# Kernel optimization log

Hardware: AMD Instinct MI355X
Metric: run time of the kernel (lower is better)

The kernel has to match this reference:

```python
import jax, jax.numpy as jnp
import numpy as np

B, S, D_IN = 4, 2048, 1024
D_OUT, H = 1024, 16
HD = D_OUT // H  # head_dim = 64

def setup_inputs() -> dict:
    key = jax.random.key(0)
    ks = jax.random.split(key, 6)
    scale_in = 1.0 / np.sqrt(D_IN)
    scale_out = 1.0 / np.sqrt(D_OUT)
    return {
        "x": jax.random.normal(ks[0], (B, S, D_IN), dtype=jnp.float32),
        "Wq": jax.random.uniform(ks[1], (D_OUT, D_IN), jnp.float32, -scale_in, scale_in),
        "Wk": jax.random.uniform(ks[2], (D_OUT, D_IN), jnp.float32, -scale_in, scale_in),
        "Wv": jax.random.uniform(ks[3], (D_OUT, D_IN), jnp.float32, -scale_in, scale_in),
        "Wo": jax.random.uniform(ks[4], (D_OUT, D_OUT), jnp.float32, -scale_out, scale_out),
        "bo": jax.random.uniform(ks[5], (D_OUT,), jnp.float32, -scale_out, scale_out),
    }

def reference(x, Wq, Wk, Wv, Wo, bo):
    b, s, _ = x.shape
    # projections (nn.Linear: x @ W.T), split into heads -> [b, h, s, hd]
    def proj(W):
        return jnp.einsum('bsd,ed->bse', x, W).reshape(b, s, H, HD).transpose(0, 2, 1, 3)
    q, k, v = proj(Wq), proj(Wk), proj(Wv)
    # full score matrix [b, h, s, s] with causal mask, scaled softmax
    scores = jnp.einsum('bhqd,bhkd->bhqk', q, k)
    causal = jnp.tril(jnp.ones((s, s), dtype=bool))
    scores = jnp.where(causal, scores, -jnp.inf)
    attn = jax.nn.softmax(scores / np.sqrt(HD), axis=-1)
    # dropout p=0.0 -> identity
    ctx = jnp.einsum('bhqk,bhkd->bqhd', attn, v).reshape(b, s, D_OUT)
    return jnp.einsum('bsd,ed->bse', ctx, Wo) + bo
```

## Files before the change

kernel.cpp:

```cpp
#include <hip/hip_runtime.h>
#include <cstdint>
#include <cstddef>

#define S_LEN   2048
#define D_MODEL 1024
#define N_HEADS 16
#define HEAD_DIM 64
#define BATCH   4
#define M_ROWS  (BATCH * S_LEN)

typedef _Float16 half8  __attribute__((ext_vector_type(8)));
typedef _Float16 half4v __attribute__((ext_vector_type(4)));
typedef float    float4v __attribute__((ext_vector_type(4)));

#define AS1 __attribute__((address_space(1)))
#define AS3 __attribute__((address_space(3)))

#define QSCL 0.1803368801111832f

__device__ __forceinline__ int swz(int row, int byteInRow) {
    return row * 128 + ((((byteInRow >> 4) ^ (row & 7)) << 4)) + (byteInRow & 15);
}

__device__ __forceinline__ int vperm(int a) {
    return (a & 0x20) | ((a & 0x0C) << 1) | ((a & 0x10) >> 2) | (a & 3);
}

__global__ __launch_bounds__(256) void cvt_all(const float* __restrict__ x,
                                               const float* __restrict__ wq,
                                               const float* __restrict__ wk,
                                               const float* __restrict__ wv,
                                               const float* __restrict__ wo,
                                               _Float16* __restrict__ dst) {
    const int NX = M_ROWS * D_MODEL / 4;
    const int NW = D_MODEL * D_MODEL / 4;
    int i = blockIdx.x * 256 + threadIdx.x;
    int j = i;
    const float4v* src;
    if (j < NX) src = (const float4v*)x;
    else {
        j -= NX;
        if (j < NW) src = (const float4v*)wq;
        else { j -= NW;
            if (j < NW) src = (const float4v*)wk;
            else { j -= NW;
                if (j < NW) src = (const float4v*)wv;
                else { j -= NW; src = (const float4v*)wo; }
            }
        }
    }
    float4v v = src[j];
    half4v h;
    h[0] = (_Float16)v[0]; h[1] = (_Float16)v[1];
    h[2] = (_Float16)v[2]; h[3] = (_Float16)v[3];
    ((half4v*)dst)[i] = h;
}

#define GK   1024
#define GNT  16
#define BUFB 49152
#define GEMM_LDS (3 * BUFB)

template <int MODE>
__global__ __launch_bounds__(512, 2) void gemm8p(const _Float16* __restrict__ A,
                                                 const _Float16* __restrict__ Bw,
                                                 _Float16* __restrict__ O1,
                                                 _Float16* __restrict__ O2,
                                                 _Float16* __restrict__ O3,
                                                 float* __restrict__ Of,
                                                 const float* __restrict__ bias,
                                                 int N) {
    extern __shared__ char smem[];

    const int tid  = threadIdx.x;
    const int wave = tid >> 6;
    const int lane = tid & 63;
    const int quad = lane >> 4;
    const int l16  = lane & 15;
    const int wm   = wave >> 1;
    const int wn   = wave & 1;

    const int rowBase = blockIdx.x * 256;
    const int colBase = blockIdx.y * 128;

    const int srow = tid >> 3;
    const int csw  = ((tid & 7) ^ (srow & 7)) * 8;
    const _Float16* aS[4];
    const _Float16* bS[2];
#pragma unroll
    for (int i = 0; i < 4; ++i)
        aS[i] = A + (size_t)(rowBase + i * 64 + srow) * GK + csw;
#pragma unroll
    for (int j = 0; j < 2; ++j)
        bS[j] = Bw + (size_t)(colBase + j * 64 + srow) * GK + csw;
    const int dstOff = tid * 16;

    auto stage = [&](int kt, int part) {
        char* base = smem + (kt % 3) * BUFB;
        const size_t ko = (size_t)kt * 64;
        if (part == 0) {
            __builtin_amdgcn_global_load_lds((const AS1 void*)(aS[0] + ko),
                (AS3 void*)(base + 0 * 8192 + dstOff), 16, 0, 0);
            __builtin_amdgcn_global_load_lds((const AS1 void*)(aS[1] + ko),
                (AS3 void*)(base + 1 * 8192 + dstOff), 16, 0, 0);
            __builtin_amdgcn_global_load_lds((const AS1 void*)(bS[0] + ko),
                (AS3 void*)(base + 32768 + dstOff), 16, 0, 0);
        } else {
            __builtin_amdgcn_global_load_lds((const AS1 void*)(aS[2] + ko),
                (AS3 void*)(base + 2 * 8192 + dstOff), 16, 0, 0);
            __builtin_amdgcn_global_load_lds((const AS1 void*)(aS[3] + ko),
                (AS3 void*)(base + 3 * 8192 + dstOff), 16, 0, 0);
            __builtin_amdgcn_global_load_lds((const AS1 void*)(bS[1] + ko),
                (AS3 void*)(base + 32768 + 8192 + dstOff), 16, 0, 0);
        }
    };

    const int aRow = (wm * 64 + l16) * 128;
    const int bRow = (wn * 64 + l16) * 128;
    int swzk[2];
    swzk[0] = ((quad)     ^ (l16 & 7)) << 4;
    swzk[1] = ((quad + 4) ^ (l16 & 7)) << 4;

    float4v acc[4][4] = {};

    stage(0, 0); stage(0, 1); stage(1, 0); stage(1, 1);
    asm volatile("s_waitcnt vmcnt(6)" ::: "memory");
    __builtin_amdgcn_s_barrier();

#pragma unroll
    for (int kt = 0; kt < GNT; ++kt) {
        const char* Ab = smem + (kt % 3) * BUFB;
        const char* Bb = Ab + 32768;
#pragma unroll
        for (int ks = 0; ks < 2; ++ks) {
            half8 af[4], bf[4];
#pragma unroll
            for (int mi = 0; mi < 4; ++mi)
                af[mi] = *(const half8*)(Ab + aRow + mi * 2048 + swzk[ks]);
#pragma unroll
            for (int ni = 0; ni < 4; ++ni)
                bf[ni] = *(const half8*)(Bb + bRow + ni * 2048 + swzk[ks]);
            if (kt + 2 < GNT) stage(kt + 2, ks);
            __builtin_amdgcn_s_barrier();
            asm volatile("s_waitcnt lgkmcnt(0)" ::: "memory");
            __builtin_amdgcn_sched_barrier(0);
            __builtin_amdgcn_s_setprio(1);
#pragma unroll
            for (int mi = 0; mi < 4; ++mi)
#pragma unroll
                for (int ni = 0; ni < 4; ++ni)
                    acc[mi][ni] = __builtin_amdgcn_mfma_f32_16x16x32_f16(
                        af[mi], bf[ni], acc[mi][ni], 0, 0, 0);
            __builtin_amdgcn_s_setprio(0);
            if (ks == 1) {
                if (kt + 2 < GNT) {
                    asm volatile("s_waitcnt vmcnt(6)" ::: "memory");
                } else if (kt + 1 < GNT) {
                    asm volatile("s_waitcnt vmcnt(0)" ::: "memory");
                }
            }
            __builtin_amdgcn_s_barrier();
        }
    }

    const int rowOff = wm * 64;
    const int colOff = wn * 64;
#pragma unroll
    for (int mi = 0; mi < 4; ++mi)
#pragma unroll
        for (int ni = 0; ni < 4; ++ni) {
            const int col = colBase + colOff + ni * 16 + l16;
#pragma unroll
            for (int i = 0; i < 4; ++i) {
                const int row = rowBase + rowOff + mi * 16 + quad * 4 + i;
                float v = acc[mi][ni][i];
                if (MODE == 0) {
                    int b_ = row >> 11, s_ = row & 2047;
                    int proj = col >> 10, d = col & 1023;
                    int h_ = d >> 6, hd = d & 63;
                    if (proj == 2) {
                        int sp = (s_ & ~63) | vperm(s_ & 63);
                        O3[(((size_t)(b_ * 16 + h_) * 64 + hd) << 11) + sp] = (_Float16)v;
                    } else {
                        _Float16* dst = proj ? O2 : O1;
                        if (proj == 0) v *= QSCL;
                        dst[(((size_t)(b_ * 16 + h_) * 2048 + s_) << 6) + hd] = (_Float16)v;
                    }
                } else {
                    Of[(size_t)row * N + col] = v + bias[col];
                }
            }
        }
}

template <bool MASKED>
__device__ __forceinline__ void qk_sm(const half8 qf[2],
                                      const _Float16* __restrict__ Ks,
                                      int krow0, int qt, int quad, int c,
                                      half8 (&pf)[2], float4v& ol, half8 ones) {
    float4v sT[4] = {};
    __builtin_amdgcn_s_setprio(1);
#pragma unroll
    for (int nt = 0; nt < 4; ++nt)
#pragma unroll
        for (int ks = 0; ks < 2; ++ks) {
            half8 kf = *(const half8*)((const char*)Ks + swz(nt * 16 + c, ks * 64 + quad * 16));
            sT[nt] = __builtin_amdgcn_mfma_f32_16x16x32_f16(kf, qf[ks], sT[nt], 0, 0, 0);
        }
    __builtin_amdgcn_s_setprio(0);

    const int qrow = qt + c;
#pragma unroll
    for (int kk = 0; kk < 2; ++kk) {
        float e[2][4];
#pragma unroll
        for (int jh = 0; jh < 2; ++jh) {
            const int nt = 2 * kk + jh;
#pragma unroll
            for (int i = 0; i < 4; ++i) {
                float ev = __builtin_amdgcn_exp2f(sT[nt][i]);
                if (MASKED)
                    ev = (krow0 + nt * 16 + quad * 4 + i <= qrow) ? ev : 0.0f;
                e[jh][i] = ev;
            }
        }
        auto p0 = __builtin_amdgcn_cvt_pkrtz(e[0][0], e[0][1]);
        auto p1 = __builtin_amdgcn_cvt_pkrtz(e[0][2], e[0][3]);
        auto p2 = __builtin_amdgcn_cvt_pkrtz(e[1][0], e[1][1]);
        auto p3 = __builtin_amdgcn_cvt_pkrtz(e[1][2], e[1][3]);
        half8 pfv;
        pfv[0] = p0[0]; pfv[1] = p0[1]; pfv[2] = p1[0]; pfv[3] = p1[1];
        pfv[4] = p2[0]; pfv[5] = p2[1]; pfv[6] = p3[0]; pfv[7] = p3[1];
        pf[kk] = pfv;
        ol = __builtin_amdgcn_mfma_f32_16x16x32_f16(pfv, ones, ol, 0, 0, 0);
    }
}

__global__ __launch_bounds__(256, 4) void attn_flash10(const _Float16* __restrict__ Q,
                                                       const _Float16* __restrict__ Kg,
                                                       const _Float16* __restrict__ Vt,
                                                       _Float16* __restrict__ Ctx) {
    __shared__ __align__(16) _Float16 Ks[2 * 64 * 64];
    __shared__ __align__(16) _Float16 Vs[2 * 64 * 64];

    const int tid  = threadIdx.x;
    const int wave = tid >> 6;
    const int lane = tid & 63;
    const int quad = lane >> 4;
    const int c    = lane & 15;

    const int h    = blockIdx.x;
    const int y    = blockIdx.y;
    const int bb   = blockIdx.z;
    const int hp   = (y < 8) ? y : 23 - y;
    const int pair = hp >> 1;
    const int hf   = hp & 1;

    const int qA   = pair * 128 + hf * 64 + wave * 16;
    const int qB   = (15 - pair) * 128 + hf * 64 + wave * 16;
    const int nkbB = (15 - pair) * 2 + hf + 1;

    const _Float16* Qb  = Q  + ((size_t)(bb * 16 + h) << 17);
    const _Float16* Kb  = Kg + ((size_t)(bb * 16 + h) << 17);
    const _Float16* Vtb = Vt + ((size_t)(bb * 16 + h) << 17);

    half8 qfA[2], qfB[2];
    {
        const _Float16* qa = Qb + (size_t)(qA + c) * 64;
        qfA[0] = *(const half8*)(qa + quad * 8);
        qfA[1] = *(const half8*)(qa + 32 + quad * 8);
        const _Float16* qb = Qb + (size_t)(qB + c) * 64;
        qfB[0] = *(const half8*)(qb + quad * 8);
        qfB[1] = *(const half8*)(qb + 32 + quad * 8);
    }

    size_t koff[2], voff[2];
#pragma unroll
    for (int it = 0; it < 2; ++it) {
        int F = it * 4096 + tid * 16;
        int r = F >> 7;
        int blk = (tid & 7) ^ (r & 7);
        koff[it] = (size_t)r * 64 + blk * 8;
        voff[it] = (size_t)r * 2048 + blk * 8;
    }

    float4v oA[4] = {}, oB[4] = {};
    float4v olA = {}, olB = {};
    half8 ones;
#pragma unroll
    for (int i = 0; i < 8; ++i) ones[i] = (_Float16)1.0f;

    auto stage = [&](int kb, int buf) {
        const size_t kbase = (size_t)kb * 64 * 64;
#pragma unroll
        for (int it = 0; it < 2; ++it) {
            __builtin_amdgcn_global_load_lds(
                (const AS1 void*)(Kb + kbase + koff[it]),
                (AS3 void*)((char*)Ks + buf * 8192 + it * 4096 + wave * 1024), 16, 0, 0);
            __builtin_amdgcn_global_load_lds(
                (const AS1 void*)(Vtb + kb * 64 + voff[it]),
                (AS3 void*)((char*)Vs + buf * 8192 + it * 4096 + wave * 1024), 16, 0, 0);
        }
    };

    stage(0, 0);
    for (int kb = 0; kb < nkbB; ++kb) {
        __syncthreads();
        if (kb + 1 < nkbB) stage(kb + 1, (kb + 1) & 1);

        const _Float16* Ksb = Ks + (kb & 1) * 4096;
        const _Float16* Vsb = Vs + (kb & 1) * 4096;
        const int krow0 = kb * 64;
        const bool aB = krow0 <= qB + 15;
        const bool aA = krow0 <= qA + 15;

        half8 pfB[2], pfA[2];
        if (aB) {
            if (krow0 + 63 <= qB)
                qk_sm<false>(qfB, Ksb, krow0, qB, quad, c, pfB, olB, ones);
            else
                qk_sm<true >(qfB, Ksb, krow0, qB, quad, c, pfB, olB, ones);
        }
        if (aA) {
            if (krow0 + 63 <= qA)
                qk_sm<false>(qfA, Ksb, krow0, qA, quad, c, pfA, olA, ones);
            else
                qk_sm<true >(qfA, Ksb, krow0, qA, quad, c, pfA, olA, ones);
        }

        __builtin_amdgcn_s_setprio(1);
#pragma unroll
        for (int kk = 0; kk < 2; ++kk)
#pragma unroll
            for (int dt = 0; dt < 4; ++dt) {
                half8 vf = *(const half8*)((const char*)Vsb + swz(dt * 16 + c, kk * 64 + quad * 16));
                if (aB)
                    oB[dt] = __builtin_amdgcn_mfma_f32_16x16x32_f16(
                        pfB[kk], vf, oB[dt], 0, 0, 0);
                if (aA)
                    oA[dt] = __builtin_amdgcn_mfma_f32_16x16x32_f16(
                        pfA[kk], vf, oA[dt], 0, 0, 0);
            }
        __builtin_amdgcn_s_setprio(0);
    }

#pragma unroll
    for (int t = 0; t < 2; ++t) {
        const int qt = t ? qB : qA;
#pragma unroll
        for (int i = 0; i < 4; ++i) {
            const float lsum = t ? olB[i] : olA[i];
            const float inv = 1.0f / lsum;
            const int row_g = qt + quad * 4 + i;
            _Float16* dst = Ctx + (size_t)(bb * 2048 + row_g) * 1024 + h * 64;
#pragma unroll
            for (int dt = 0; dt < 4; ++dt) {
                const float ov = t ? oB[dt][i] : oA[dt][i];
                dst[dt * 16 + c] = (_Float16)(ov * inv);
            }
        }
    }
}

extern "C" void kernel_launch(void* const* d_in, const int* in_sizes, int n_in,
                              void* d_out, int out_size, void* d_ws, size_t ws_size,
                              hipStream_t stream) {
    const float* x  = (const float*)d_in[0];
    const float* Wq = (const float*)d_in[1];
    const float* Wk = (const float*)d_in[2];
    const float* Wv = (const float*)d_in[3];
    const float* Wo = (const float*)d_in[4];
    const float* bo = (const float*)d_in[5];
    float* out = (float*)d_out;

    _Float16* Xh   = (_Float16*)d_ws;
    _Float16* Wqkvh = Xh + (size_t)M_ROWS * D_MODEL;
    _Float16* Woh  = Wqkvh + (size_t)3 * D_MODEL * D_MODEL;
    _Float16* Qh   = Woh + (size_t)D_MODEL * D_MODEL;
    _Float16* Kh   = Qh + (size_t)M_ROWS * D_MODEL;
    _Float16* Vth  = Kh + (size_t)M_ROWS * D_MODEL;
    _Float16* Ch   = Vth + (size_t)M_ROWS * D_MODEL;

    static bool s_init = false;
    if (!s_init) {
        hipFuncSetAttribute((const void*)gemm8p<0>,
                            hipFuncAttributeMaxDynamicSharedMemorySize, GEMM_LDS);
        hipFuncSetAttribute((const void*)gemm8p<2>,
                            hipFuncAttributeMaxDynamicSharedMemorySize, GEMM_LDS);
        s_init = true;
    }

    const int TOT4 = (M_ROWS * D_MODEL + 4 * D_MODEL * D_MODEL) / 4;
    cvt_all<<<TOT4 / 256, 256, 0, stream>>>(x, Wq, Wk, Wv, Wo, Xh);

    gemm8p<0><<<dim3(M_ROWS / 256, 3072 / 128), 512, GEMM_LDS, stream>>>(
        Xh, Wqkvh, Qh, Kh, Vth, nullptr, nullptr, 3072);

    attn_flash10<<<dim3(N_HEADS, 16, BATCH), 256, 0, stream>>>(Qh, Kh, Vth, Ch);

    gemm8p<2><<<dim3(M_ROWS / 256, D_MODEL / 128), 512, GEMM_LDS, stream>>>(
        Ch, Woh, nullptr, nullptr, nullptr, out, bo, D_MODEL);
}
```

Baseline: 164.5 us.

## Enlarge GEMM tiles to 256x256 with four-phase double-buffered pipeline

Replaces the 256x128 triple-buffered GEMM with a 256x256 tile, double-buffered in LDS (128 KB), with each k-tile split into four sub-phases that interleave partial loads of the next tile with MFMA work. Each wave now holds a 128x64 accumulator (8x4 fragments), roughly doubling operand reuse per LDS read and halving global traffic for the weight side. This costs more accumulator registers and allows only one block per CU at 128 KB LDS. The grid also shrinks, so the output projection launches only 128 blocks, which may underfill the CUs.

```diff
diff --git a/kernel.cpp b/kernel.cpp
--- a/kernel.cpp
+++ b/kernel.cpp
@@ -56,20 +56,61 @@
     ((half4v*)dst)[i] = h;
 }
 
-#define GK   1024
-#define GNT  16
-#define BUFB 49152
-#define GEMM_LDS (3 * BUFB)
+#define GK    1024
+#define GNT   16
+#define GBUF  65536
+#define G2LDS 131072
+
+#define VMC(N) asm volatile("s_waitcnt vmcnt(" #N ")" ::: "memory")
+
+#define GPHASE(MH, NH, STAGE)                                                     \
+    {                                                                             \
+        half8 af[4][2], bf[2][2];                                                 \
+        _Pragma("unroll")                                                         \
+        for (int mi = 0; mi < 4; ++mi) {                                          \
+            af[mi][0] = *(const half8*)(Ab + (MH)*16384 + aWOff + mi*2048 + swzk0);\
+            af[mi][1] = *(const half8*)(Ab + (MH)*16384 + aWOff + mi*2048 + swzk1);\
+        }                                                                         \
+        _Pragma("unroll")                                                         \
+        for (int ni = 0; ni < 2; ++ni) {                                          \
+            bf[ni][0] = *(const half8*)(Ab + (NH)*16384 + bWOff + ni*2048 + swzk0);\
+            bf[ni][1] = *(const half8*)(Ab + (NH)*16384 + bWOff + ni*2048 + swzk1);\
+        }                                                                         \
+        STAGE;                                                                    \
+        __builtin_amdgcn_s_barrier();                                             \
+        asm volatile("s_waitcnt lgkmcnt(0)" ::: "memory");                        \
+        __builtin_amdgcn_sched_barrier(0);                                        \
+        __builtin_amdgcn_s_setprio(1);                                            \
+        _Pragma("unroll")                                                         \
+        for (int mi = 0; mi < 4; ++mi)                                            \
+            _Pragma("unroll")                                                     \
+            for (int ni = 0; ni < 2; ++ni) {                                      \
+                acc[(MH)*4+mi][(NH)*2+ni] = __builtin_amdgcn_mfma_f32_16x16x32_f16(\
+                    af[mi][0], bf[ni][0], acc[(MH)*4+mi][(NH)*2+ni], 0, 0, 0);    \
+                acc[(MH)*4+mi][(NH)*2+ni] = __builtin_amdgcn_mfma_f32_16x16x32_f16(\
+                    af[mi][1], bf[ni][1], acc[(MH)*4+mi][(NH)*2+ni], 0, 0, 0);    \
+            }                                                                     \
+        __builtin_amdgcn_s_setprio(0);                                            \
+    }
+
+#define GKTILE(KT, S0, S1, S2, S3, W0, W3)                                        \
+    {                                                                             \
+        const char* Ab = smem + ((KT) & 1) * GBUF;                                \
+        GPHASE(0, 0, S0); W0; __builtin_amdgcn_s_barrier();                       \
+        GPHASE(0, 1, S1);     __builtin_amdgcn_s_barrier();                       \
+        GPHASE(1, 0, S2);     __builtin_amdgcn_s_barrier();                       \
+        GPHASE(1, 1, S3); W3; __builtin_amdgcn_s_barrier();                       \
+    }
 
 template <int MODE>
-__global__ __launch_bounds__(512, 2) void gemm8p(const _Float16* __restrict__ A,
-                                                 const _Float16* __restrict__ Bw,
-                                                 _Float16* __restrict__ O1,
-                                                 _Float16* __restrict__ O2,
-                                                 _Float16* __restrict__ O3,
-                                                 float* __restrict__ Of,
-                                                 const float* __restrict__ bias,
-                                                 int N) {
+__global__ __launch_bounds__(512, 2) void gemm256(const _Float16* __restrict__ A,
+                                                  const _Float16* __restrict__ Bw,
+                                                  _Float16* __restrict__ O1,
+                                                  _Float16* __restrict__ O2,
+                                                  _Float16* __restrict__ O3,
+                                                  float* __restrict__ Of,
+                                                  const float* __restrict__ bias,
+                                                  int N) {
     extern __shared__ char smem[];
 
     const int tid  = threadIdx.x;
@@ -77,102 +118,65 @@
     const int lane = tid & 63;
     const int quad = lane >> 4;
     const int l16  = lane & 15;
-    const int wm   = wave >> 1;
-    const int wn   = wave & 1;
+    const int wm   = wave >> 2;
+    const int wn   = wave & 3;
 
     const int rowBase = blockIdx.x * 256;
-    const int colBase = blockIdx.y * 128;
-
-    const int srow = tid >> 3;
-    const int csw  = ((tid & 7) ^ (srow & 7)) * 8;
-    const _Float16* aS[4];
-    const _Float16* bS[2];
-#pragma unroll
-    for (int i = 0; i < 4; ++i)
-        aS[i] = A + (size_t)(rowBase + i * 64 + srow) * GK + csw;
-#pragma unroll
-    for (int j = 0; j < 2; ++j)
-        bS[j] = Bw + (size_t)(colBase + j * 64 + srow) * GK + csw;
+    const int colBase = blockIdx.y * 256;
+
+    const int r   = tid >> 3;
+    const int csw = ((tid & 7) ^ (r & 7)) * 8;
+    const _Float16* aBase = A  + (size_t)(rowBase + r) * GK + csw;
+    const _Float16* bBase = Bw + (size_t)(colBase + (r >> 5) * 64 + (r & 31)) * GK + csw;
     const int dstOff = tid * 16;
 
-    auto stage = [&](int kt, int part) {
-        char* base = smem + (kt % 3) * BUFB;
-        const size_t ko = (size_t)kt * 64;
-        if (part == 0) {
-            __builtin_amdgcn_global_load_lds((const AS1 void*)(aS[0] + ko),
-                (AS3 void*)(base + 0 * 8192 + dstOff), 16, 0, 0);
-            __builtin_amdgcn_global_load_lds((const AS1 void*)(aS[1] + ko),
-                (AS3 void*)(base + 1 * 8192 + dstOff), 16, 0, 0);
-            __builtin_amdgcn_global_load_lds((const AS1 void*)(bS[0] + ko),
-                (AS3 void*)(base + 32768 + dstOff), 16, 0, 0);
-        } else {
-            __builtin_amdgcn_global_load_lds((const AS1 void*)(aS[2] + ko),
-                (AS3 void*)(base + 2 * 8192 + dstOff), 16, 0, 0);
-            __builtin_amdgcn_global_load_lds((const AS1 void*)(aS[3] + ko),
-                (AS3 void*)(base + 3 * 8192 + dstOff), 16, 0, 0);
-            __builtin_amdgcn_global_load_lds((const AS1 void*)(bS[1] + ko),
-                (AS3 void*)(base + 32768 + 8192 + dstOff), 16, 0, 0);
-        }
+    auto stageA = [&](int kt, int mh) {
+        char* dst = smem + (kt & 1) * GBUF + mh * 16384 + dstOff;
+        const _Float16* src = aBase + (size_t)mh * 64 * GK + (size_t)kt * 64;
+        __builtin_amdgcn_global_load_lds((const AS1 void*)src,
+                                         (AS3 void*)dst, 16, 0, 0);
+        __builtin_amdgcn_global_load_lds((const AS1 void*)(src + (size_t)128 * GK),
+                                         (AS3 void*)(dst + 8192), 16, 0, 0);
     };
-
-    const int aRow = (wm * 64 + l16) * 128;
-    const int bRow = (wn * 64 + l16) * 128;
-    int swzk[2];
-    swzk[0] = ((quad)     ^ (l16 & 7)) << 4;
-    swzk[1] = ((quad + 4) ^ (l16 & 7)) << 4;
-
-    float4v acc[4][4] = {};
-
-    stage(0, 0); stage(0, 1); stage(1, 0); stage(1, 1);
-    asm volatile("s_waitcnt vmcnt(6)" ::: "memory");
+    auto stageB = [&](int kt, int nh) {
+        char* dst = smem + (kt & 1) * GBUF + 32768 + nh * 16384 + dstOff;
+        const _Float16* src = bBase + (size_t)nh * 32 * GK + (size_t)kt * 64;
+        __builtin_amdgcn_global_load_lds((const AS1 void*)src,
+                                         (AS3 void*)dst, 16, 0, 0);
+        __builtin_amdgcn_global_load_lds((const AS1 void*)(src + (size_t)128 * GK),
+                                         (AS3 void*)(dst + 8192), 16, 0, 0);
+    };
+
+    const int swzk0 = ((quad)     ^ (l16 & 7)) << 4;
+    const int swzk1 = ((quad + 4) ^ (l16 & 7)) << 4;
+    const int aWOff = wm * 8192 + l16 * 128;
+    const int bWOff = 32768 + wn * 4096 + l16 * 128;
+
+    float4v acc[8][4] = {};
+
+    stageA(0, 0); stageB(0, 0); stageA(0, 1); stageB(0, 1); stageA(1, 0); stageB(1, 0);
+    VMC(8);
     __builtin_amdgcn_s_barrier();
 
-#pragma unroll
-    for (int kt = 0; kt < GNT; ++kt) {
-        const char* Ab = smem + (kt % 3) * BUFB;
-        const char* Bb = Ab + 32768;
-#pragma unroll
-        for (int ks = 0; ks < 2; ++ks) {
-            half8 af[4], bf[4];
-#pragma unroll
-            for (int mi = 0; mi < 4; ++mi)
-                af[mi] = *(const half8*)(Ab + aRow + mi * 2048 + swzk[ks]);
-#pragma unroll
-            for (int ni = 0; ni < 4; ++ni)
-                bf[ni] = *(const half8*)(Bb + bRow + ni * 2048 + swzk[ks]);
-            if (kt + 2 < GNT) stage(kt + 2, ks);
-            __builtin_amdgcn_s_barrier();
-            asm volatile("s_waitcnt lgkmcnt(0)" ::: "memory");
-            __builtin_amdgcn_sched_barrier(0);
-            __builtin_amdgcn_s_setprio(1);
-#pragma unroll
-            for (int mi = 0; mi < 4; ++mi)
-#pragma unroll
-                for (int ni = 0; ni < 4; ++ni)
-                    acc[mi][ni] = __builtin_amdgcn_mfma_f32_16x16x32_f16(
-                        af[mi], bf[ni], acc[mi][ni], 0, 0, 0);
-            __builtin_amdgcn_s_setprio(0);
-            if (ks == 1) {
-                if (kt + 2 < GNT) {
-                    asm volatile("s_waitcnt vmcnt(6)" ::: "memory");
-                } else if (kt + 1 < GNT) {
-                    asm volatile("s_waitcnt vmcnt(0)" ::: "memory");
-                }
-            }
-            __builtin_amdgcn_s_barrier();
-        }
-    }
-
-    const int rowOff = wm * 64;
-    const int colOff = wn * 64;
-#pragma unroll
-    for (int mi = 0; mi < 4; ++mi)
+    for (int ktp = 0; ktp < 7; ++ktp) {
+        const int kt = 2 * ktp;
+        GKTILE(kt,     stageA(kt + 1, 1), stageB(kt + 1, 1),
+                       stageA(kt + 2, 0), stageB(kt + 2, 0), VMC(6), VMC(8));
+        GKTILE(kt + 1, stageA(kt + 2, 1), stageB(kt + 2, 1),
+                       stageA(kt + 3, 0), stageB(kt + 3, 0), VMC(6), VMC(8));
+    }
+    GKTILE(14, stageA(15, 1), stageB(15, 1), , , VMC(6), VMC(4));
+    GKTILE(15, , , , , VMC(0), );
+
+#pragma unroll
+    for (int mi = 0; mi < 8; ++mi)
 #pragma unroll
         for (int ni = 0; ni < 4; ++ni) {
-            const int col = colBase + colOff + ni * 16 + l16;
+            const int col = colBase + wn * 64 + (ni >> 1) * 32 + (ni & 1) * 16 + l16;
 #pragma unroll
             for (int i = 0; i < 4; ++i) {
-                const int row = rowBase + rowOff + mi * 16 + quad * 4 + i;
+                const int row = rowBase + wm * 128 + (mi >> 2) * 64 + (mi & 3) * 16
+                                + quad * 4 + i;
                 float v = acc[mi][ni][i];
                 if (MODE == 0) {
                     int b_ = row >> 11, s_ = row & 2047;
@@ -278,10 +282,10 @@
 #pragma unroll
     for (int it = 0; it < 2; ++it) {
         int F = it * 4096 + tid * 16;
-        int r = F >> 7;
-        int blk = (tid & 7) ^ (r & 7);
-        koff[it] = (size_t)r * 64 + blk * 8;
-        voff[it] = (size_t)r * 2048 + blk * 8;
+        int rr = F >> 7;
+        int blk = (tid & 7) ^ (rr & 7);
+        koff[it] = (size_t)rr * 64 + blk * 8;
+        voff[it] = (size_t)rr * 2048 + blk * 8;
     }
 
     float4v oA[4] = {}, oB[4] = {};
@@ -373,31 +377,31 @@
     const float* bo = (const float*)d_in[5];
     float* out = (float*)d_out;
 
-    _Float16* Xh   = (_Float16*)d_ws;
+    _Float16* Xh    = (_Float16*)d_ws;
     _Float16* Wqkvh = Xh + (size_t)M_ROWS * D_MODEL;
-    _Float16* Woh  = Wqkvh + (size_t)3 * D_MODEL * D_MODEL;
-    _Float16* Qh   = Woh + (size_t)D_MODEL * D_MODEL;
-    _Float16* Kh   = Qh + (size_t)M_ROWS * D_MODEL;
-    _Float16* Vth  = Kh + (size_t)M_ROWS * D_MODEL;
-    _Float16* Ch   = Vth + (size_t)M_ROWS * D_MODEL;
+    _Float16* Woh   = Wqkvh + (size_t)3 * D_MODEL * D_MODEL;
+    _Float16* Qh    = Woh + (size_t)D_MODEL * D_MODEL;
+    _Float16* Kh    = Qh + (size_t)M_ROWS * D_MODEL;
+    _Float16* Vth   = Kh + (size_t)M_ROWS * D_MODEL;
+    _Float16* Ch    = Vth + (size_t)M_ROWS * D_MODEL;
 
     static bool s_init = false;
     if (!s_init) {
-        hipFuncSetAttribute((const void*)gemm8p<0>,
-                            hipFuncAttributeMaxDynamicSharedMemorySize, GEMM_LDS);
-        hipFuncSetAttribute((const void*)gemm8p<2>,
-                            hipFuncAttributeMaxDynamicSharedMemorySize, GEMM_LDS);
+        hipFuncSetAttribute((const void*)gemm256<0>,
+                            hipFuncAttributeMaxDynamicSharedMemorySize, G2LDS);
+        hipFuncSetAttribute((const void*)gemm256<2>,
+                            hipFuncAttributeMaxDynamicSharedMemorySize, G2LDS);
         s_init = true;
     }
 
     const int TOT4 = (M_ROWS * D_MODEL + 4 * D_MODEL * D_MODEL) / 4;
     cvt_all<<<TOT4 / 256, 256, 0, stream>>>(x, Wq, Wk, Wv, Wo, Xh);
 
-    gemm8p<0><<<dim3(M_ROWS / 256, 3072 / 128), 512, GEMM_LDS, stream>>>(
+    gemm256<0><<<dim3(M_ROWS / 256, 3072 / 256), 512, G2LDS, stream>>>(
         Xh, Wqkvh, Qh, Kh, Vth, nullptr, nullptr, 3072);
 
     attn_flash10<<<dim3(N_HEADS, 16, BATCH), 256, 0, stream>>>(Qh, Kh, Vth, Ch);
 
-    gemm8p<2><<<dim3(M_ROWS / 256, D_MODEL / 128), 512, GEMM_LDS, stream>>>(
+    gemm256<2><<<dim3(M_ROWS / 256, D_MODEL / 256), 512, G2LDS, stream>>>(
         Ch, Woh, nullptr, nullptr, nullptr, out, bo, D_MODEL);
 }
```

Measured after the change: 196.8 us. 1.2x slower.
